# Optimization experiments

Measured on AMD Instinct MI355X. Metric: run time of the kernel, lower is better.

## Reference

```python
import jax, jax.numpy as jnp
import numpy as np
import math

D_MODEL = 1024
NHEAD = 16
D_K = D_MODEL // NHEAD
B, S = 2, 2048


def setup_inputs() -> dict:
    key = jax.random.key(0)
    ks = jax.random.split(key, 9)
    x = jax.random.normal(ks[0], (B, S, D_MODEL), dtype=jnp.float32)
    # causal mask, broadcastable to (B, nhead, S, S); 0 entries are masked out
    mask = jnp.tril(jnp.ones((S, S), dtype=jnp.int32))[None, None, :, :]
    scale = 1.0 / math.sqrt(D_MODEL)
    def lin(kw, kb):
        W = jax.random.uniform(kw, (D_MODEL, D_MODEL), dtype=jnp.float32, minval=-scale, maxval=scale)
        b = jax.random.uniform(kb, (D_MODEL,), dtype=jnp.float32, minval=-scale, maxval=scale)
        return W, b
    Wq, bq = lin(ks[1], ks[2])
    Wk, bk = lin(ks[3], ks[4])
    Wv, bv = lin(ks[5], ks[6])
    Wo, bo = lin(ks[7], ks[8])
    return {"x": x, "mask": mask, "Wq": Wq, "bq": bq, "Wk": Wk, "bk": bk,
            "Wv": Wv, "bv": bv, "Wo": Wo, "bo": bo}


def reference(x, mask, Wq, bq, Wk, bk, Wv, bv, Wo, bo):
    b, s, _ = x.shape
    def heads(W, bias):
        # (b, s, d_model) @ (d_model, d_model) -> (b, nhead, s, d_k)
        return (x @ W.T + bias).reshape(b, s, NHEAD, D_K).transpose(0, 2, 1, 3)
    Q, K, V = heads(Wq, bq), heads(Wk, bk), heads(Wv, bv)
    scores = jnp.einsum('bhqd,bhkd->bhqk', Q, K) / math.sqrt(D_K)
    scores = jnp.where(mask == 0, jnp.float32(-1e9), scores)
    attn = jax.nn.softmax(scores, axis=-1)  # dropout is identity in eval mode
    out = jnp.einsum('bhqk,bhkd->bhqd', attn, V)
    out = out.transpose(0, 2, 1, 3).reshape(b, s, D_MODEL)
    return out @ Wo.T + bo
```

## Files before the change

kernel.cpp:

```cpp
#include <hip/hip_runtime.h>
#include <hip/hip_bf16.h>

#define DMODEL 1024
#define NH     16
#define DKH    64
#define BSZ    2
#define SEQ    2048
#define MROWS  (BSZ*SEQ)
#define WELEM  (DMODEL*DMODEL)

typedef __attribute__((ext_vector_type(8))) short short8;
typedef __attribute__((ext_vector_type(4))) float f32x4;

__device__ __forceinline__ ushort f2bf(float f) {
    return __bfloat16_as_ushort(__float2bfloat16(f));
}
__device__ __forceinline__ unsigned pk2(float lo, float hi) {
    return (unsigned)f2bf(lo) | ((unsigned)f2bf(hi) << 16);
}
__device__ __forceinline__ void load_lds16(const ushort* g, ushort* l) {
    __builtin_amdgcn_global_load_lds(
        (const __attribute__((address_space(1))) unsigned int*)g,
        (__attribute__((address_space(3))) unsigned int*)l, 16, 0, 0);
}

__global__ __launch_bounds__(256)
void cvt_all(const float* __restrict__ x,
             const float* __restrict__ W0, const float* __restrict__ W1,
             const float* __restrict__ W2, const float* __restrict__ W3,
             ushort* __restrict__ xbf, ushort* __restrict__ Wcat,
             ushort* __restrict__ Wo)
{
    const int blk = blockIdx.x;
    const float* src;
    ushort* dst;
    int base;
    if (blk < 2048)      { src = x;  dst = xbf;             base = blk * 2048; }
    else if (blk < 2560) { src = W0; dst = Wcat;            base = (blk - 2048) * 2048; }
    else if (blk < 3072) { src = W1; dst = Wcat + WELEM;    base = (blk - 2560) * 2048; }
    else if (blk < 3584) { src = W2; dst = Wcat + 2*WELEM;  base = (blk - 3072) * 2048; }
    else                 { src = W3; dst = Wo;              base = (blk - 3584) * 2048; }
    const size_t off = (size_t)base + threadIdx.x * 8;
    const float4 f0 = *(const float4*)(src + off);
    const float4 f1 = *(const float4*)(src + off + 4);
    uint4 o;
    o.x = pk2(f0.x, f0.y); o.y = pk2(f0.z, f0.w);
    o.z = pk2(f1.x, f1.y); o.w = pk2(f1.z, f1.w);
    *(uint4*)(dst + off) = o;
}

__global__ __launch_bounds__(256)
void gemm_qkv(const ushort* __restrict__ xbf, const ushort* __restrict__ Wcat,
              const float* __restrict__ bq, const float* __restrict__ bk,
              const float* __restrict__ bv,
              ushort* __restrict__ Qh, ushort* __restrict__ Kh,
              ushort* __restrict__ VT)
{
    __shared__ ushort Ash[128][32];
    __shared__ ushort Bsh[128][32];

    const int t    = threadIdx.x;
    const int m0   = blockIdx.y * 128, n0 = blockIdx.x * 128;
    const int wave = t >> 6;
    const int lane = t & 63;
    const int wr   = (wave >> 1) * 64;
    const int wc   = (wave & 1) * 64;
    const int quad = lane >> 4;
    const int r16  = lane & 15;

    const int row0 = wave * 16 + (lane >> 2);
    const int row1 = 64 + wave * 16 + (lane >> 2);
    const int ch   = (lane & 3) * 8;

    f32x4 acc[4][4];
    #pragma unroll
    for (int i = 0; i < 4; ++i)
        #pragma unroll
        for (int j = 0; j < 4; ++j)
            acc[i][j] = (f32x4){0.f, 0.f, 0.f, 0.f};

    for (int k0 = 0; k0 < DMODEL; k0 += 32) {
        load_lds16(xbf  + (size_t)(m0 + row0) * DMODEL + k0 + ch, &Ash[wave * 16][0]);
        load_lds16(xbf  + (size_t)(m0 + row1) * DMODEL + k0 + ch, &Ash[64 + wave * 16][0]);
        load_lds16(Wcat + (size_t)(n0 + row0) * DMODEL + k0 + ch, &Bsh[wave * 16][0]);
        load_lds16(Wcat + (size_t)(n0 + row1) * DMODEL + k0 + ch, &Bsh[64 + wave * 16][0]);
        __syncthreads();

        short8 af[4], bf[4];
        #pragma unroll
        for (int i = 0; i < 4; ++i) af[i] = *(const short8*)&Ash[wr + i * 16 + r16][quad * 8];
        #pragma unroll
        for (int j = 0; j < 4; ++j) bf[j] = *(const short8*)&Bsh[wc + j * 16 + r16][quad * 8];

        #pragma unroll
        for (int i = 0; i < 4; ++i)
            #pragma unroll
            for (int j = 0; j < 4; ++j)
                acc[i][j] = __builtin_amdgcn_mfma_f32_16x16x32_bf16(af[i], bf[j], acc[i][j], 0, 0, 0);
        __syncthreads();
    }

    const int region = n0 >> 10;
    const float* bp  = (region == 0) ? bq : (region == 1) ? bk : bv;
    ushort* outQK    = (region == 0) ? Qh : Kh;
    const float osc  = (region == 0) ? 0.125f : 1.0f;
    const int nbase  = n0 & 1023;

    #pragma unroll
    for (int i = 0; i < 4; ++i) {
        #pragma unroll
        for (int j = 0; j < 4; ++j) {
            #pragma unroll
            for (int reg = 0; reg < 4; ++reg) {
                const int m  = m0 + wr + i * 16 + quad * 4 + reg;
                const int n  = nbase + wc + j * 16 + r16;
                const float v = (acc[i][j][reg] + bp[n]) * osc;
                const int b = m >> 11, s = m & (SEQ - 1);
                const int h = n >> 6,  dk = n & 63;
                if (region < 2) {
                    outQK[((size_t)(b * NH + h) * SEQ + s) * DKH + dk] = f2bf(v);
                } else {
                    VT[(((size_t)(b * NH + h)) * DKH + dk) * SEQ + s] = f2bf(v);
                }
            }
        }
    }
}

__global__ __launch_bounds__(256)
void gemm_out(const ushort* __restrict__ O, const ushort* __restrict__ Wo,
              const float* __restrict__ bo, float* __restrict__ out)
{
    __shared__ ushort Ash[128][32];
    __shared__ ushort Bsh[64][32];

    const int t    = threadIdx.x;
    const int m0   = blockIdx.y * 128, n0 = blockIdx.x * 64;
    const int wave = t >> 6;
    const int lane = t & 63;
    const int wr   = (wave >> 1) * 64;
    const int wc   = (wave & 1) * 32;
    const int quad = lane >> 4;
    const int r16  = lane & 15;

    const int row0 = wave * 16 + (lane >> 2);
    const int row1 = 64 + wave * 16 + (lane >> 2);
    const int ch   = (lane & 3) * 8;

    f32x4 acc[4][2];
    #pragma unroll
    for (int i = 0; i < 4; ++i)
        #pragma unroll
        for (int j = 0; j < 2; ++j)
            acc[i][j] = (f32x4){0.f, 0.f, 0.f, 0.f};

    for (int k0 = 0; k0 < DMODEL; k0 += 32) {
        const int ma0 = m0 + row0, ma1 = m0 + row1;
        load_lds16(O + ((size_t)(ma0 >> 11) * NH + (k0 >> 6)) * (SEQ * DKH)
                     + (size_t)(ma0 & (SEQ - 1)) * DKH + (k0 & 63) + ch,
                   &Ash[wave * 16][0]);
        load_lds16(O + ((size_t)(ma1 >> 11) * NH + (k0 >> 6)) * (SEQ * DKH)
                     + (size_t)(ma1 & (SEQ - 1)) * DKH + (k0 & 63) + ch,
                   &Ash[64 + wave * 16][0]);
        load_lds16(Wo + (size_t)(n0 + row0) * DMODEL + k0 + ch, &Bsh[wave * 16][0]);
        __syncthreads();

        short8 af[4], bf[2];
        #pragma unroll
        for (int i = 0; i < 4; ++i) af[i] = *(const short8*)&Ash[wr + i * 16 + r16][quad * 8];
        #pragma unroll
        for (int j = 0; j < 2; ++j) bf[j] = *(const short8*)&Bsh[wc + j * 16 + r16][quad * 8];

        #pragma unroll
        for (int i = 0; i < 4; ++i)
            #pragma unroll
            for (int j = 0; j < 2; ++j)
                acc[i][j] = __builtin_amdgcn_mfma_f32_16x16x32_bf16(af[i], bf[j], acc[i][j], 0, 0, 0);
        __syncthreads();
    }

    #pragma unroll
    for (int i = 0; i < 4; ++i) {
        #pragma unroll
        for (int j = 0; j < 2; ++j) {
            #pragma unroll
            for (int reg = 0; reg < 4; ++reg) {
                const int m = m0 + wr + i * 16 + quad * 4 + reg;
                const int n = n0 + wc + j * 16 + r16;
                out[(size_t)m * DMODEL + n] = acc[i][j][reg] + bo[n];
            }
        }
    }
}

__global__ __launch_bounds__(256)
void gemm_mfma(const void* __restrict__ A, const void* __restrict__ W,
               const float* __restrict__ bias, void* __restrict__ out,
               int amode, int bmode, int outmode, float oscale)
{
    __shared__ ushort Ash[128][40];
    __shared__ ushort Bsh[128][40];

    const int t    = threadIdx.x;
    const int m0   = blockIdx.y * 128, n0 = blockIdx.x * 128;
    const int srow = t >> 1;
    const int shal = (t & 1) * 16;

    const int wave = t >> 6;
    const int lane = t & 63;
    const int wr   = (wave >> 1) * 64;
    const int wc   = (wave & 1) * 64;
    const int quad = lane >> 4;
    const int r16  = lane & 15;

    f32x4 acc[4][4];
    #pragma unroll
    for (int i = 0; i < 4; ++i)
        #pragma unroll
        for (int j = 0; j < 4; ++j)
            acc[i][j] = (f32x4){0.f, 0.f, 0.f, 0.f};

    for (int k0 = 0; k0 < DMODEL; k0 += 32) {
        uint4 a01, a23, b01, b23;
        if (amode == 0) {
            const float* ap = (const float*)A + (size_t)(m0 + srow) * DMODEL + k0 + shal;
            const float4 f0 = *(const float4*)(ap);
            const float4 f1 = *(const float4*)(ap + 4);
            const float4 f2 = *(const float4*)(ap + 8);
            const float4 f3 = *(const float4*)(ap + 12);
            a01 = (uint4){pk2(f0.x,f0.y), pk2(f0.z,f0.w), pk2(f1.x,f1.y), pk2(f1.z,f1.w)};
            a23 = (uint4){pk2(f2.x,f2.y), pk2(f2.z,f2.w), pk2(f3.x,f3.y), pk2(f3.z,f3.w)};
        } else if (amode == 1) {
            const int m = m0 + srow;
            const ushort* ap = (const ushort*)A
                + ((size_t)(m >> 11) * NH + (k0 >> 6)) * (SEQ * DKH)
                + (size_t)(m & (SEQ - 1)) * DKH + (k0 & 63) + shal;
            a01 = *(const uint4*)(ap);
            a23 = *(const uint4*)(ap + 8);
        } else {
            const ushort* ap = (const ushort*)A + (size_t)(m0 + srow) * DMODEL + k0 + shal;
            a01 = *(const uint4*)(ap);
            a23 = *(const uint4*)(ap + 8);
        }
        if (bmode == 0) {
            const float* wp = (const float*)W + (size_t)(n0 + srow) * DMODEL + k0 + shal;
            const float4 w0 = *(const float4*)(wp);
            const float4 w1 = *(const float4*)(wp + 4);
            const float4 w2 = *(const float4*)(wp + 8);
            const float4 w3 = *(const float4*)(wp + 12);
            b01 = (uint4){pk2(w0.x,w0.y), pk2(w0.z,w0.w), pk2(w1.x,w1.y), pk2(w1.z,w1.w)};
            b23 = (uint4){pk2(w2.x,w2.y), pk2(w2.z,w2.w), pk2(w3.x,w3.y), pk2(w3.z,w3.w)};
        } else {
            const ushort* wp = (const ushort*)W + (size_t)(n0 + srow) * DMODEL + k0 + shal;
            b01 = *(const uint4*)(wp);
            b23 = *(const uint4*)(wp + 8);
        }

        *(uint4*)&Ash[srow][shal]     = a01;
        *(uint4*)&Ash[srow][shal + 8] = a23;
        *(uint4*)&Bsh[srow][shal]     = b01;
        *(uint4*)&Bsh[srow][shal + 8] = b23;
        __syncthreads();

        short8 af[4], bf[4];
        #pragma unroll
        for (int i = 0; i < 4; ++i) af[i] = *(const short8*)&Ash[wr + i * 16 + r16][quad * 8];
        #pragma unroll
        for (int j = 0; j < 4; ++j) bf[j] = *(const short8*)&Bsh[wc + j * 16 + r16][quad * 8];

        #pragma unroll
        for (int i = 0; i < 4; ++i)
            #pragma unroll
            for (int j = 0; j < 4; ++j)
                acc[i][j] = __builtin_amdgcn_mfma_f32_16x16x32_bf16(af[i], bf[j], acc[i][j], 0, 0, 0);
        __syncthreads();
    }

    #pragma unroll
    for (int i = 0; i < 4; ++i) {
        #pragma unroll
        for (int j = 0; j < 4; ++j) {
            #pragma unroll
            for (int reg = 0; reg < 4; ++reg) {
                const int m = m0 + wr + i * 16 + quad * 4 + reg;
                const int n = n0 + wc + j * 16 + r16;
                const float v = (acc[i][j][reg] + bias[n]) * oscale;
                if (outmode == 0) {
                    ((float*)out)[(size_t)m * DMODEL + n] = v;
                } else if (outmode == 1) {
                    ((ushort*)out)[((size_t)(m >> 11) * NH + (n >> 6)) * (SEQ * DKH)
                                   + (size_t)(m & (SEQ - 1)) * DKH + (n & 63)] = f2bf(v);
                } else {
                    ((ushort*)out)[(((size_t)(m >> 11) * NH + (n >> 6)) * DKH + (n & 63)) * SEQ
                                   + (m & (SEQ - 1))] = f2bf(v);
                }
            }
        }
    }
}

__global__ __launch_bounds__(256)
void attn_flash(ushort* __restrict__ Qh,
                const ushort* __restrict__ Kh,
                const ushort* __restrict__ VT)
{
    __shared__ ushort Kl[128][72];
    __shared__ ushort Vl[64][136];
    __shared__ ushort Pl[4][16][136];

    const int t256 = threadIdx.x;
    const int wave = t256 >> 6;
    const int lane = t256 & 63;
    const int quad = lane >> 4;
    const int r16  = lane & 15;

    const int slot = blockIdx.x & 7;
    const int bh   = slot * 4 + ((blockIdx.x >> 3) & 3);
    const int qt   = blockIdx.x >> 5;
    const int q0   = qt * 64;

    ushort*       Qbase = Qh + (size_t)bh * SEQ * DKH;
    const ushort* Kbase = Kh + (size_t)bh * SEQ * DKH;
    const ushort* Vbase = VT + (size_t)bh * DKH * SEQ;

    short8 qf[2];
    {
        const ushort* qrow = Qbase + (size_t)(q0 + wave * 16 + r16) * DKH;
        qf[0] = *(const short8*)(qrow + quad * 8);
        qf[1] = *(const short8*)(qrow + 32 + quad * 8);
    }

    f32x4 oacc[4];
    #pragma unroll
    for (int i = 0; i < 4; ++i) oacc[i] = (f32x4){0.f, 0.f, 0.f, 0.f};
    float lpart[4] = {0.f, 0.f, 0.f, 0.f};

    const int T   = (qt >> 1) + 1;
    const int off = (qt & 1) * 64;

    for (int t = 0; t < T; ++t) {
        {
            const int krow = t256 >> 1, kc = (t256 & 1) * 32;
            const ushort* kg = Kbase + (size_t)(t * 128 + krow) * DKH + kc;
            *(uint4*)&Kl[krow][kc]      = *(const uint4*)(kg);
            *(uint4*)&Kl[krow][kc + 8]  = *(const uint4*)(kg + 8);
            *(uint4*)&Kl[krow][kc + 16] = *(const uint4*)(kg + 16);
            *(uint4*)&Kl[krow][kc + 24] = *(const uint4*)(kg + 24);
            const int vrow = t256 >> 2, vc = (t256 & 3) * 32;
            const ushort* vg = Vbase + (size_t)vrow * SEQ + t * 128 + vc;
            *(uint4*)&Vl[vrow][vc]      = *(const uint4*)(vg);
            *(uint4*)&Vl[vrow][vc + 8]  = *(const uint4*)(vg + 8);
            *(uint4*)&Vl[vrow][vc + 16] = *(const uint4*)(vg + 16);
            *(uint4*)&Vl[vrow][vc + 24] = *(const uint4*)(vg + 24);
        }
        __syncthreads();

        f32x4 sacc[8];
        #pragma unroll
        for (int nt = 0; nt < 8; ++nt) {
            sacc[nt] = (f32x4){0.f, 0.f, 0.f, 0.f};
            short8 b0 = *(const short8*)&Kl[nt * 16 + r16][quad * 8];
            short8 b1 = *(const short8*)&Kl[nt * 16 + r16][32 + quad * 8];
            sacc[nt] = __builtin_amdgcn_mfma_f32_16x16x32_bf16(qf[0], b0, sacc[nt], 0, 0, 0);
            sacc[nt] = __builtin_amdgcn_mfma_f32_16x16x32_bf16(qf[1], b1, sacc[nt], 0, 0, 0);
        }

        const bool diag = (t == T - 1);
        #pragma unroll
        for (int reg = 0; reg < 4; ++reg) {
            const int row_local = wave * 16 + quad * 4 + reg + off;
            #pragma unroll
            for (int nt = 0; nt < 8; ++nt) {
                float pv = __expf(sacc[nt][reg]);
                if (diag && (nt * 16 + r16) > row_local) pv = 0.f;
                lpart[reg] += pv;
                Pl[wave][quad * 4 + reg][nt * 16 + r16] = f2bf(pv);
            }
        }

        #pragma unroll
        for (int c = 0; c < 4; ++c) {
            short8 af = *(const short8*)&Pl[wave][r16][c * 32 + quad * 8];
            #pragma unroll
            for (int ct = 0; ct < 4; ++ct) {
                short8 bf = *(const short8*)&Vl[ct * 16 + r16][c * 32 + quad * 8];
                oacc[ct] = __builtin_amdgcn_mfma_f32_16x16x32_bf16(af, bf, oacc[ct], 0, 0, 0);
            }
        }
        __syncthreads();
    }

    #pragma unroll
    for (int reg = 0; reg < 4; ++reg)
        for (int d = 1; d < 16; d <<= 1)
            lpart[reg] += __shfl_xor(lpart[reg], d, 64);

    #pragma unroll
    for (int reg = 0; reg < 4; ++reg) {
        const float inv = 1.f / lpart[reg];
        const int q = q0 + wave * 16 + quad * 4 + reg;
        ushort* orow = Qbase + (size_t)q * DKH;
        #pragma unroll
        for (int ct = 0; ct < 4; ++ct)
            orow[ct * 16 + r16] = f2bf(oacc[ct][reg] * inv);
    }
}

extern "C" void kernel_launch(void* const* d_in, const int* in_sizes, int n_in,
                              void* d_out, int out_size, void* d_ws, size_t ws_size,
                              hipStream_t stream)
{
    const float* x  = (const float*)d_in[0];
    const float* Wf[4] = {(const float*)d_in[2], (const float*)d_in[4],
                          (const float*)d_in[6], (const float*)d_in[8]};
    const float* Bf[4] = {(const float*)d_in[3], (const float*)d_in[5],
                          (const float*)d_in[7], (const float*)d_in[9]};

    const size_t HSZ = (size_t)MROWS * DMODEL;
    ushort* Qh = (ushort*)d_ws;
    ushort* Kh = (ushort*)d_out;
    ushort* VT = (ushort*)d_out + HSZ;

    const dim3 blk(256);

    if (ws_size >= 24u * 1024 * 1024) {
        ushort* Wcat = Qh + HSZ;
        ushort* Wo   = Wcat + 3 * (size_t)WELEM;
        ushort* xbf  = Wo + WELEM;

        cvt_all<<<dim3(4096), blk, 0, stream>>>(x, Wf[0], Wf[1], Wf[2], Wf[3],
                                                xbf, Wcat, Wo);

        gemm_qkv<<<dim3(3 * DMODEL / 128, MROWS / 128), blk, 0, stream>>>(
            xbf, Wcat, Bf[0], Bf[1], Bf[2], Qh, Kh, VT);

        attn_flash<<<dim3(BSZ * NH * 32), blk, 0, stream>>>(Qh, Kh, VT);

        gemm_out<<<dim3(DMODEL / 64, MROWS / 128), blk, 0, stream>>>(
            Qh, Wo, Bf[3], (float*)d_out);
    } else {
        const dim3 gg(DMODEL / 128, MROWS / 128);
        gemm_mfma<<<gg, blk, 0, stream>>>(x, Wf[0], Bf[0], Qh, 0, 0, 1, 0.125f);
        gemm_mfma<<<gg, blk, 0, stream>>>(x, Wf[1], Bf[1], Kh, 0, 0, 1, 1.0f);
        gemm_mfma<<<gg, blk, 0, stream>>>(x, Wf[2], Bf[2], VT, 0, 0, 2, 1.0f);
        attn_flash<<<dim3(BSZ * NH * 32), blk, 0, stream>>>(Qh, Kh, VT);
        gemm_mfma<<<gg, blk, 0, stream>>>(Qh, Wf[3], Bf[3], d_out, 1, 0, 0, 1.0f);
    }
}
```

Before: 214.3 us.

## Prefetch next K/V tile into registers and transpose score MFMA in attention

The attention loop now loads the next K/V tile from global memory into registers while the current tile is being computed, so load latency overlaps with MFMA work. The score MFMA operands are swapped so each lane holds one query row. That allows packed 64-bit P stores to LDS and a single running row-sum reduced with two shuffles instead of a full butterfly. Q is pre-scaled by log2(e)/8 so the exponential can use the native exp2, and s_setprio raises wave priority around the MFMA phases. The costs are more registers for the prefetch buffers, which may lower occupancy, and one extra shuffle per output row.

```diff
diff --git a/kernel.cpp b/kernel.cpp
--- a/kernel.cpp
+++ b/kernel.cpp
@@ -103,7 +103,7 @@
     const int region = n0 >> 10;
     const float* bp  = (region == 0) ? bq : (region == 1) ? bk : bv;
     ushort* outQK    = (region == 0) ? Qh : Kh;
-    const float osc  = (region == 0) ? 0.125f : 1.0f;
+    const float osc  = (region == 0) ? 0.18033688f : 1.0f;
     const int nbase  = n0 & 1023;
 
     #pragma unroll
@@ -333,51 +333,83 @@
     f32x4 oacc[4];
     #pragma unroll
     for (int i = 0; i < 4; ++i) oacc[i] = (f32x4){0.f, 0.f, 0.f, 0.f};
-    float lpart[4] = {0.f, 0.f, 0.f, 0.f};
-
-    const int T   = (qt >> 1) + 1;
-    const int off = (qt & 1) * 64;
+    float lsum = 0.f;
+
+    const int T    = (qt >> 1) + 1;
+    const int off  = (qt & 1) * 64;
+    const int qrel = off + wave * 16 + r16;
+
+    const int krow = t256 >> 1, kc = (t256 & 1) * 32;
+    const int vrow = t256 >> 2, vc = (t256 & 3) * 32;
+    const ushort* kg0 = Kbase + (size_t)krow * DKH + kc;
+    const ushort* vg0 = Vbase + (size_t)vrow * SEQ + vc;
+
+    uint4 kr0, kr1, kr2, kr3, vr0, vr1, vr2, vr3;
+    {
+        kr0 = *(const uint4*)(kg0);
+        kr1 = *(const uint4*)(kg0 + 8);
+        kr2 = *(const uint4*)(kg0 + 16);
+        kr3 = *(const uint4*)(kg0 + 24);
+        vr0 = *(const uint4*)(vg0);
+        vr1 = *(const uint4*)(vg0 + 8);
+        vr2 = *(const uint4*)(vg0 + 16);
+        vr3 = *(const uint4*)(vg0 + 24);
+    }
 
     for (int t = 0; t < T; ++t) {
-        {
-            const int krow = t256 >> 1, kc = (t256 & 1) * 32;
-            const ushort* kg = Kbase + (size_t)(t * 128 + krow) * DKH + kc;
-            *(uint4*)&Kl[krow][kc]      = *(const uint4*)(kg);
-            *(uint4*)&Kl[krow][kc + 8]  = *(const uint4*)(kg + 8);
-            *(uint4*)&Kl[krow][kc + 16] = *(const uint4*)(kg + 16);
-            *(uint4*)&Kl[krow][kc + 24] = *(const uint4*)(kg + 24);
-            const int vrow = t256 >> 2, vc = (t256 & 3) * 32;
-            const ushort* vg = Vbase + (size_t)vrow * SEQ + t * 128 + vc;
-            *(uint4*)&Vl[vrow][vc]      = *(const uint4*)(vg);
-            *(uint4*)&Vl[vrow][vc + 8]  = *(const uint4*)(vg + 8);
-            *(uint4*)&Vl[vrow][vc + 16] = *(const uint4*)(vg + 16);
-            *(uint4*)&Vl[vrow][vc + 24] = *(const uint4*)(vg + 24);
-        }
-        __syncthreads();
+        *(uint4*)&Kl[krow][kc]      = kr0;
+        *(uint4*)&Kl[krow][kc + 8]  = kr1;
+        *(uint4*)&Kl[krow][kc + 16] = kr2;
+        *(uint4*)&Kl[krow][kc + 24] = kr3;
+        *(uint4*)&Vl[vrow][vc]      = vr0;
+        *(uint4*)&Vl[vrow][vc + 8]  = vr1;
+        *(uint4*)&Vl[vrow][vc + 16] = vr2;
+        *(uint4*)&Vl[vrow][vc + 24] = vr3;
+        __syncthreads();
+
+        if (t + 1 < T) {
+            const ushort* kg = kg0 + (size_t)(t + 1) * 128 * DKH;
+            kr0 = *(const uint4*)(kg);
+            kr1 = *(const uint4*)(kg + 8);
+            kr2 = *(const uint4*)(kg + 16);
+            kr3 = *(const uint4*)(kg + 24);
+            const ushort* vg = vg0 + (size_t)(t + 1) * 128;
+            vr0 = *(const uint4*)(vg);
+            vr1 = *(const uint4*)(vg + 8);
+            vr2 = *(const uint4*)(vg + 16);
+            vr3 = *(const uint4*)(vg + 24);
+        }
 
         f32x4 sacc[8];
+        __builtin_amdgcn_s_setprio(1);
         #pragma unroll
         for (int nt = 0; nt < 8; ++nt) {
-            sacc[nt] = (f32x4){0.f, 0.f, 0.f, 0.f};
             short8 b0 = *(const short8*)&Kl[nt * 16 + r16][quad * 8];
             short8 b1 = *(const short8*)&Kl[nt * 16 + r16][32 + quad * 8];
-            sacc[nt] = __builtin_amdgcn_mfma_f32_16x16x32_bf16(qf[0], b0, sacc[nt], 0, 0, 0);
-            sacc[nt] = __builtin_amdgcn_mfma_f32_16x16x32_bf16(qf[1], b1, sacc[nt], 0, 0, 0);
-        }
+            sacc[nt] = (f32x4){0.f, 0.f, 0.f, 0.f};
+            sacc[nt] = __builtin_amdgcn_mfma_f32_16x16x32_bf16(b0, qf[0], sacc[nt], 0, 0, 0);
+            sacc[nt] = __builtin_amdgcn_mfma_f32_16x16x32_bf16(b1, qf[1], sacc[nt], 0, 0, 0);
+        }
+        __builtin_amdgcn_s_setprio(0);
 
         const bool diag = (t == T - 1);
         #pragma unroll
-        for (int reg = 0; reg < 4; ++reg) {
-            const int row_local = wave * 16 + quad * 4 + reg + off;
-            #pragma unroll
-            for (int nt = 0; nt < 8; ++nt) {
-                float pv = __expf(sacc[nt][reg]);
-                if (diag && (nt * 16 + r16) > row_local) pv = 0.f;
-                lpart[reg] += pv;
-                Pl[wave][quad * 4 + reg][nt * 16 + r16] = f2bf(pv);
+        for (int nt = 0; nt < 8; ++nt) {
+            float pv[4];
+            #pragma unroll
+            for (int reg = 0; reg < 4; ++reg) {
+                float e = __builtin_amdgcn_exp2f(sacc[nt][reg]);
+                if (diag && (nt * 16 + quad * 4 + reg) > qrel) e = 0.f;
+                pv[reg] = e;
+                lsum += e;
             }
-        }
-
+            uint2 w;
+            w.x = pk2(pv[0], pv[1]);
+            w.y = pk2(pv[2], pv[3]);
+            *(uint2*)&Pl[wave][r16][nt * 16 + quad * 4] = w;
+        }
+
+        __builtin_amdgcn_s_setprio(1);
         #pragma unroll
         for (int c = 0; c < 4; ++c) {
             short8 af = *(const short8*)&Pl[wave][r16][c * 32 + quad * 8];
@@ -387,17 +419,16 @@
                 oacc[ct] = __builtin_amdgcn_mfma_f32_16x16x32_bf16(af, bf, oacc[ct], 0, 0, 0);
             }
         }
-        __syncthreads();
-    }
-
-    #pragma unroll
-    for (int reg = 0; reg < 4; ++reg)
-        for (int d = 1; d < 16; d <<= 1)
-            lpart[reg] += __shfl_xor(lpart[reg], d, 64);
+        __builtin_amdgcn_s_setprio(0);
+        __syncthreads();
+    }
+
+    lsum += __shfl_xor(lsum, 16, 64);
+    lsum += __shfl_xor(lsum, 32, 64);
 
     #pragma unroll
     for (int reg = 0; reg < 4; ++reg) {
-        const float inv = 1.f / lpart[reg];
+        const float inv = 1.f / __shfl(lsum, quad * 4 + reg, 64);
         const int q = q0 + wave * 16 + quad * 4 + reg;
         ushort* orow = Qbase + (size_t)q * DKH;
         #pragma unroll
@@ -440,7 +471,7 @@
             Qh, Wo, Bf[3], (float*)d_out);
     } else {
         const dim3 gg(DMODEL / 128, MROWS / 128);
-        gemm_mfma<<<gg, blk, 0, stream>>>(x, Wf[0], Bf[0], Qh, 0, 0, 1, 0.125f);
+        gemm_mfma<<<gg, blk, 0, stream>>>(x, Wf[0], Bf[0], Qh, 0, 0, 1, 0.18033688f);
         gemm_mfma<<<gg, blk, 0, stream>>>(x, Wf[1], Bf[1], Kh, 0, 0, 1, 1.0f);
         gemm_mfma<<<gg, blk, 0, stream>>>(x, Wf[2], Bf[2], VT, 0, 0, 2, 1.0f);
         attn_flash<<<dim3(BSZ * NH * 32), blk, 0, stream>>>(Qh, Kh, VT);
```

New measurement: 200.1 us. 1.07x faster.
